# Performance work log

Measured on AMD Instinct MI355X. Metric: run time of the kernel, lower is better.

## Reference

```python
import jax, jax.numpy as jnp
import numpy as np

D = 512; PE = 64; H = 8; DH = 64; INNER = H * DH; FF = 4 * D
B = 2; L = 2048; K = 32; G = 128; LT = L + G
SCALE = DH ** -0.5


def _ln(x, g, b):
    m = jnp.mean(x, -1, keepdims=True)
    v = jnp.var(x, -1, keepdims=True)
    return (x - m) * jax.lax.rsqrt(v + 1e-5) * g + b


def _heads(x):
    b, n, _ = x.shape
    return x.reshape(b, n, H, DH).transpose(0, 2, 1, 3)


def _merge(x):
    b, _, n, _ = x.shape
    return x.transpose(0, 2, 1, 3).reshape(b, n, INNER)


def _cross(q_in, ctx, wq, wk, wv, wo, bo):
    Q = _heads(q_in @ wq); Kh = _heads(ctx @ wk); V = _heads(ctx @ wv)
    a = jax.nn.softmax(jnp.einsum('bhnd,bhmd->bhnm', Q, Kh) * SCALE, axis=-1)
    return _merge(jnp.einsum('bhnm,bhmd->bhnd', a, V)) @ wo + bo


def _ffn(x, w1, b1, w2, b2):
    return jax.nn.gelu(x @ w1 + b1, approximate=False) @ w2 + b2


def setup_inputs():
    key = jax.random.key(0)
    ks = jax.random.split(key, 40)
    w = lambda k, shape: jax.random.normal(k, shape, jnp.float32) * 0.02
    return dict(
        latents=jax.random.normal(ks[0], (B, LT, D), jnp.float32),
        rpe=jax.random.normal(ks[1], (B, L, K, PE), jnp.float32),
        distances=jax.random.uniform(ks[2], (B, L, K), jnp.float32) * 10.0,
        sn_g=jnp.ones((D,), jnp.float32), sn_b=jnp.zeros((D,), jnp.float32),
        la_wq=w(ks[3], (D, INNER)), la_wk=w(ks[4], (D + PE, INNER)), la_wv=w(ks[5], (D + PE, INNER)),
        la_wo=w(ks[6], (INNER, D)), la_bo=jnp.zeros((D,), jnp.float32),
        log_sigma=jnp.full((H,), float(np.log(3.0)), jnp.float32),
        scn_g=jnp.ones((D,), jnp.float32), scn_b=jnp.zeros((D,), jnp.float32),
        s2g_wq=w(ks[7], (D, INNER)), s2g_wk=w(ks[8], (D, INNER)), s2g_wv=w(ks[9], (D, INNER)),
        s2g_wo=w(ks[10], (INNER, D)), s2g_bo=jnp.zeros((D,), jnp.float32),
        gcn_g=jnp.ones((D,), jnp.float32), gcn_b=jnp.zeros((D,), jnp.float32),
        g2s_wq=w(ks[11], (D, INNER)), g2s_wk=w(ks[12], (D, INNER)), g2s_wv=w(ks[13], (D, INNER)),
        g2s_wo=w(ks[14], (INNER, D)), g2s_bo=jnp.zeros((D,), jnp.float32),
        gfn_g=jnp.ones((D,), jnp.float32), gfn_b=jnp.zeros((D,), jnp.float32),
        gff_w1=w(ks[15], (D, FF)), gff_b1=jnp.zeros((FF,), jnp.float32),
        gff_w2=w(ks[16], (FF, D)), gff_b2=jnp.zeros((D,), jnp.float32),
        sfn_g=jnp.ones((D,), jnp.float32), sfn_b=jnp.zeros((D,), jnp.float32),
        sff_w1=w(ks[17], (D, FF)), sff_b1=jnp.zeros((FF,), jnp.float32),
        sff_w2=w(ks[18], (FF, D)), sff_b2=jnp.zeros((D,), jnp.float32),
        topk_indices=jax.random.randint(ks[19], (B, L, K), 0, L),
        num_spatial=L,
    )


def _forward(latents, rpe, distances, sn_g, sn_b, la_wq, la_wk, la_wv, la_wo, la_bo, log_sigma,
             scn_g, scn_b, s2g_wq, s2g_wk, s2g_wv, s2g_wo, s2g_bo,
             gcn_g, gcn_b, g2s_wq, g2s_wk, g2s_wv, g2s_wo, g2s_bo,
             gfn_g, gfn_b, gff_w1, gff_b1, gff_w2, gff_b2,
             sfn_g, sfn_b, sff_w1, sff_b1, sff_w2, sff_b2,
             topk_indices, num_spatial):
    spatial = latents[:, :num_spatial]
    glob = latents[:, num_spatial:]
    b, l, _ = spatial.shape
    k = topk_indices.shape[-1]
    # 1) local self-attention: kNN gather + RPE concat + Gaussian distance bias
    xn = _ln(spatial, sn_g, sn_b)
    neighbors = jax.vmap(lambda xb, ib: xb[ib])(xn, topk_indices)      # [B, L, k, D]
    ctx = jnp.concatenate([neighbors, rpe], axis=-1)                   # [B, L, k, D+PE]
    Q = _heads(xn @ la_wq)                                             # [B, H, L, DH]
    Kt = (ctx @ la_wk).reshape(b, l, k, H, DH).transpose(0, 3, 1, 2, 4)
    Vt = (ctx @ la_wv).reshape(b, l, k, H, DH).transpose(0, 3, 1, 2, 4)
    attn = jnp.einsum('bhld,bhlkd->bhlk', Q, Kt) * SCALE
    sigma_sq = jnp.exp(2.0 * log_sigma)[None, :, None, None]           # sigma**2 per head
    attn = attn - (distances ** 2)[:, None] / (2.0 * sigma_sq)
    attn = jax.nn.softmax(attn, axis=-1)
    o = jnp.einsum('bhlk,bhlkd->bhld', attn, Vt)
    spatial = spatial + (_merge(o) @ la_wo + la_bo)
    # 2) spatial -> global, 3) global -> spatial, global FFN
    spatial = spatial + _cross(_ln(spatial, scn_g, scn_b), glob, s2g_wq, s2g_wk, s2g_wv, s2g_wo, s2g_bo)
    glob = glob + _cross(_ln(glob, gcn_g, gcn_b), spatial, g2s_wq, g2s_wk, g2s_wv, g2s_wo, g2s_bo)
    glob = glob + _ffn(_ln(glob, gfn_g, gfn_b), gff_w1, gff_b1, gff_w2, gff_b2)
    # 4) spatial FFN
    spatial = spatial + _ffn(_ln(spatial, sfn_g, sfn_b), sff_w1, sff_b1, sff_w2, sff_b2)
    return jnp.concatenate([spatial, glob], axis=1)


def reference(latents, rpe, distances, sn_g, sn_b, la_wq, la_wk, la_wv, la_wo, la_bo, log_sigma,
              scn_g, scn_b, s2g_wq, s2g_wk, s2g_wv, s2g_wo, s2g_bo,
              gcn_g, gcn_b, g2s_wq, g2s_wk, g2s_wv, g2s_wo, g2s_bo,
              gfn_g, gfn_b, gff_w1, gff_b1, gff_w2, gff_b2,
              sfn_g, sfn_b, sff_w1, sff_b1, sff_w2, sff_b2,
              topk_indices, num_spatial):
    return _forward(latents, rpe, distances, sn_g, sn_b, la_wq, la_wk, la_wv, la_wo, la_bo, log_sigma,
                    scn_g, scn_b, s2g_wq, s2g_wk, s2g_wv, s2g_wo, s2g_bo,
                    gcn_g, gcn_b, g2s_wq, g2s_wk, g2s_wv, g2s_wo, g2s_bo,
                    gfn_g, gfn_b, gff_w1, gff_b1, gff_w2, gff_b2,
                    sfn_g, sfn_b, sff_w1, sff_b1, sff_w2, sff_b2,
                    topk_indices, num_spatial)
```

## Files before the change

kernel.cpp:

```cpp
#include <hip/hip_runtime.h>
#include <math.h>

namespace {
constexpr int D = 512;
constexpr int PE = 64;
constexpr int H = 8;
constexpr int DH = 64;
constexpr int INNER = 512;
constexpr int FF = 2048;
constexpr int B = 2;
constexpr int L = 2048;
constexpr int KN = 32;
constexpr int G = 128;
constexpr int LT = L + G;
constexpr float SCALE = 0.125f;

typedef unsigned short u16;
typedef unsigned short u16x8 __attribute__((ext_vector_type(8)));
typedef float f32x4 __attribute__((ext_vector_type(4)));
typedef _Float16 h2 __attribute__((ext_vector_type(2)));

#if defined(__has_builtin)
#if __has_builtin(__builtin_amdgcn_fdot2)
#define HAVE_FDOT2 1
#endif
#endif

__device__ __forceinline__ u16 f2bf(float x) {
  union { float f; unsigned u; } v;
  v.f = x;
  unsigned r = v.u + 0x7fffu + ((v.u >> 16) & 1u);
  return (u16)(r >> 16);
}

__device__ __forceinline__ float bf2f(u16 x) {
  union { unsigned u; float f; } v;
  v.u = ((unsigned)x) << 16;
  return v.f;
}

__device__ __forceinline__ u16 f2h(float x) {
  _Float16 h = (_Float16)x;
  return *(u16*)&h;
}

__device__ __forceinline__ unsigned pack2bf(float a, float b) {
  return (unsigned)f2bf(a) | ((unsigned)f2bf(b) << 16);
}

__device__ __forceinline__ float gelu_exact(float x) {
  return 0.5f * x * (1.0f + erff(x * 0.7071067811865475f));
}

__device__ __forceinline__ f32x4 mfma_16x16x32_bf16(u16x8 a, u16x8 b, f32x4 c) {
  asm("v_mfma_f32_16x16x32_bf16 %0, %1, %2, %0" : "+v"(c) : "v"(a), "v"(b));
  return c;
}

__device__ __forceinline__ float dot2h(h2 a, h2 b, float c) {
#ifdef HAVE_FDOT2
  return __builtin_amdgcn_fdot2(a, b, c, false);
#else
  return c + (float)a[0] * (float)b[0] + (float)a[1] * (float)b[1];
#endif
}

__device__ __forceinline__ void gload_lds16(const u16* g, const u16* lds_base) {
  __builtin_amdgcn_global_load_lds(
      (const __attribute__((address_space(1))) unsigned int*)(uintptr_t)g,
      (__attribute__((address_space(3))) unsigned int*)(unsigned)(uintptr_t)lds_base,
      16, 0, 0);
}

__global__ __launch_bounds__(256) void split_kernel(const float* __restrict__ latents,
                                                    float* __restrict__ sp, float* __restrict__ gl) {
  int i = blockIdx.x * 256 + threadIdx.x;
  const int total = B * LT * D / 4;
  if (i >= total) return;
  float4 v = ((const float4*)latents)[i];
  int fi = i * 4;
  int d = fi % D;
  int row = fi / D;
  int l = row % LT;
  int b = row / LT;
  if (l < L) ((float4*)sp)[((size_t)(b * L + l) * D + d) / 4] = v;
  else ((float4*)gl)[((size_t)(b * G + (l - L)) * D + d) / 4] = v;
}

__global__ __launch_bounds__(256) void assemble_kernel(const float* __restrict__ sp,
                                                       const float* __restrict__ gl,
                                                       float* __restrict__ out) {
  int i = blockIdx.x * 256 + threadIdx.x;
  const int total = B * LT * D / 4;
  if (i >= total) return;
  int fi = i * 4;
  int d = fi % D;
  int row = fi / D;
  int l = row % LT;
  int b = row / LT;
  float4 v;
  if (l < L) v = ((const float4*)sp)[((size_t)(b * L + l) * D + d) / 4];
  else v = ((const float4*)gl)[((size_t)(b * G + (l - L)) * D + d) / 4];
  ((float4*)out)[i] = v;
}

__global__ __launch_bounds__(256) void ln_kernel(const float* __restrict__ in,
                                                 const float* __restrict__ gw,
                                                 const float* __restrict__ bw,
                                                 u16* __restrict__ out) {
  int row = blockIdx.x;
  int t = threadIdx.x;
  const float* x = in + (size_t)row * D;
  float2 v = ((const float2*)x)[t];
  float s = v.x + v.y;
  float sq = v.x * v.x + v.y * v.y;
#pragma unroll
  for (int m = 1; m < 64; m <<= 1) {
    s += __shfl_xor(s, m, 64);
    sq += __shfl_xor(sq, m, 64);
  }
  __shared__ float ss[4], s2[4];
  int w = t >> 6;
  if ((t & 63) == 0) { ss[w] = s; s2[w] = sq; }
  __syncthreads();
  s = ss[0] + ss[1] + ss[2] + ss[3];
  sq = s2[0] + s2[1] + s2[2] + s2[3];
  float mean = s * (1.0f / D);
  float var = sq * (1.0f / D) - mean * mean;
  float rs = rsqrtf(var + 1e-5f);
  float2 gv = ((const float2*)gw)[t];
  float2 bv = ((const float2*)bw)[t];
  float ox = (v.x - mean) * rs * gv.x + bv.x;
  float oy = (v.y - mean) * rs * gv.y + bv.y;
  ((unsigned*)(out + (size_t)row * D))[t] = pack2bf(ox, oy);
}

__global__ __launch_bounds__(256) void cvt_bf16_kernel(const float* __restrict__ in,
                                                       u16* __restrict__ out, int n4) {
  int i = blockIdx.x * 256 + threadIdx.x;
  if (i >= n4) return;
  float4 v = ((const float4*)in)[i];
  ushort4 o;
  o.x = f2bf(v.x); o.y = f2bf(v.y); o.z = f2bf(v.z); o.w = f2bf(v.w);
  ((ushort4*)out)[i] = o;
}

struct WtJob { const float* src; u16* dst; int K; int N; int off; int dstride; };
struct WtJobs { WtJob j[16]; };

__global__ __launch_bounds__(256) void wt_convert_kernel(WtJobs jobs) {
  __shared__ float tile[32][33];
  int bid = blockIdx.x;
  int e = 0;
#pragma unroll
  for (int i = 1; i < 16; ++i) if (bid >= jobs.j[i].off) e = i;
  const WtJob& J = jobs.j[e];
  int ti = bid - J.off;
  int tiles_n = J.N >> 5;
  int tk = ti / tiles_n, tn = ti - tk * tiles_n;
  int t = threadIdx.x;
  int r = t >> 3, c4 = (t & 7) * 4;
  float4 v = *(const float4*)&J.src[(size_t)(tk * 32 + r) * J.N + tn * 32 + c4];
  tile[r][c4 + 0] = v.x; tile[r][c4 + 1] = v.y; tile[r][c4 + 2] = v.z; tile[r][c4 + 3] = v.w;
  __syncthreads();
  int r2 = t >> 3, k4 = (t & 7) * 4;
  ushort4 o;
  o.x = f2bf(tile[k4 + 0][r2]);
  o.y = f2bf(tile[k4 + 1][r2]);
  o.z = f2bf(tile[k4 + 2][r2]);
  o.w = f2bf(tile[k4 + 3][r2]);
  *(ushort4*)&J.dst[(size_t)(tn * 32 + r2) * J.dstride + tk * 32 + k4] = o;
}

__global__ __launch_bounds__(256) void comp_qt_kernel(const float* __restrict__ wq,
                                                      const float* __restrict__ wkb,
                                                      u16* __restrict__ out) {
  int h = blockIdx.x, ct = blockIdx.y;
  __shared__ float wk_s[64][68];
  __shared__ float wq_s[64][68];
  int t = threadIdx.x;
  int r = t >> 4, c4 = (t & 15) * 4;
#pragma unroll
  for (int i = 0; i < 4; ++i) {
    int rr = r + i * 16;
    *(float4*)&wk_s[rr][c4] = *(const float4*)&wkb[(size_t)rr * INNER + h * DH + c4];
    *(float4*)&wq_s[rr][c4] = *(const float4*)&wq[(size_t)(ct * 64 + rr) * INNER + h * DH + c4];
  }
  __syncthreads();
  int p = t >> 2, cb = (t & 3) * 16;
  float acc[16] = {};
  for (int d = 0; d < 64; ++d) {
    float a = wk_s[p][d];
#pragma unroll
    for (int j = 0; j < 16; ++j) acc[j] += a * wq_s[cb + j][d];
  }
  for (int j = 0; j < 16; ++j)
    out[(size_t)(h * 64 + p) * INNER + ct * 64 + cb + j] = f2bf(acc[j]);
}

__global__ __launch_bounds__(256) void comp_wo_kernel(const float* __restrict__ la_wo,
                                                      const float* __restrict__ wvb,
                                                      u16* __restrict__ WO2t) {
  int h = blockIdx.x, jt = blockIdx.y;
  __shared__ float lo_s[64][68];
  __shared__ float wv_s[64][68];
  int t = threadIdx.x;
  int r = t >> 4, c4 = (t & 15) * 4;
#pragma unroll
  for (int i = 0; i < 4; ++i) {
    int rr = r + i * 16;
    *(float4*)&lo_s[rr][c4] = *(const float4*)&la_wo[(size_t)(h * DH + rr) * D + jt * 64 + c4];
    *(float4*)&wv_s[rr][c4] = *(const float4*)&wvb[(size_t)rr * INNER + h * DH + c4];
  }
  __syncthreads();
  int j = t >> 2, pb = (t & 3) * 16;
  float acc[16] = {};
  for (int d = 0; d < 64; ++d) {
    float a = lo_s[d][j];
#pragma unroll
    for (int i = 0; i < 16; ++i) acc[i] += a * wv_s[pb + i][d];
  }
  for (int i = 0; i < 16; ++i)
    WO2t[(size_t)(jt * 64 + j) * 1024 + 512 + h * DH + pb + i] = f2bf(acc[i]);
}

struct WSet { const u16* W[4]; void* out[4]; };

template <int BM, int BN>
__global__ __launch_bounds__(256) void gemm_v3_kernel(const u16* __restrict__ A, WSet gs,
                                                      const float* __restrict__ bias,
                                                      const float* __restrict__ res,
                                                      u16* __restrict__ out_bf,
                                                      int M, int K, int N, int act, unsigned obf) {
  constexpr int FM = BM / 32;
  constexpr int FN = BN / 32;
  __shared__ u16 As[2][BM * 64];
  __shared__ u16 Bs[2][BN * 64];
  int t = threadIdx.x;
  int wave = __builtin_amdgcn_readfirstlane(t >> 6);
  int lane = t & 63;
  int wr = wave >> 1, wc = wave & 1;
  int row16 = lane & 15, katom = lane >> 4;
  int bm = blockIdx.y * BM, bn = blockIdx.x * BN;
  const u16* W = gs.W[blockIdx.z];
  void* outp = gs.out[blockIdx.z];
  unsigned obz = (obf >> (blockIdx.z * 2)) & 3u;
  int srow = lane >> 3;
  int sg = lane & 7;
  int swz = row16 & 7;
  f32x4 acc[FM][FN] = {};

  auto stage = [&](int buf, int kb) {
#pragma unroll
    for (int c = 0; c < BM / 32; ++c) {
      int rowbase = wave * (BM / 4) + c * 8;
      int row = rowbase + srow;
      int gsrc = sg ^ (row & 7);
      gload_lds16(&A[(size_t)(bm + row) * K + kb + gsrc * 8], &As[buf][rowbase * 64]);
    }
#pragma unroll
    for (int c = 0; c < BN / 32; ++c) {
      int rowbase = wave * (BN / 4) + c * 8;
      int row = rowbase + srow;
      int gsrc = sg ^ (row & 7);
      gload_lds16(&W[(size_t)(bn + row) * K + kb + gsrc * 8], &Bs[buf][rowbase * 64]);
    }
  };

  stage(0, 0);
  __syncthreads();
  int nk = K >> 6;
  int cur = 0;
  for (int ti = 0; ti < nk; ++ti) {
    u16x8 af[2][FM], bf[2][FN];
#pragma unroll
    for (int kk = 0; kk < 2; ++kk) {
#pragma unroll
      for (int m = 0; m < FM; ++m) {
        int r = wr * (BM / 2) + m * 16 + row16;
        af[kk][m] = *(u16x8*)&As[cur][r * 64 + ((kk * 4 + katom) ^ swz) * 8];
      }
#pragma unroll
      for (int n = 0; n < FN; ++n) {
        int r = wc * (BN / 2) + n * 16 + row16;
        bf[kk][n] = *(u16x8*)&Bs[cur][r * 64 + ((kk * 4 + katom) ^ swz) * 8];
      }
    }
    __builtin_amdgcn_sched_barrier(0);
    if (ti + 1 < nk) stage(cur ^ 1, (ti + 1) << 6);
#pragma unroll
    for (int kk = 0; kk < 2; ++kk)
#pragma unroll
      for (int m = 0; m < FM; ++m)
#pragma unroll
        for (int n = 0; n < FN; ++n)
          acc[m][n] = mfma_16x16x32_bf16(af[kk][m], bf[kk][n], acc[m][n]);
    __syncthreads();
    cur ^= 1;
  }
#pragma unroll
  for (int m = 0; m < FM; ++m) {
    int row = bm + wr * (BM / 2) + m * 16 + katom * 4;
#pragma unroll
    for (int n = 0; n < FN; ++n) {
      int col = bn + wc * (BN / 2) + n * 16 + row16;
      float bsv = bias ? bias[col] : 0.f;
#pragma unroll
      for (int r = 0; r < 4; ++r) {
        float v = acc[m][n][r] + bsv;
        if (act) v = gelu_exact(v);
        size_t oi = (size_t)(row + r) * N + col;
        if (res) v += res[oi];
        if (obz == 1) ((u16*)outp)[oi] = f2bf(v);
        else if (obz == 3) ((u16*)outp)[oi] = f2h(v);
        else {
          ((float*)outp)[oi] = v;
          if (obz == 2) out_bf[oi] = f2bf(v);
        }
      }
    }
  }
}

__global__ __launch_bounds__(256) void local_attn2_kernel(
    const u16* __restrict__ Qh, const u16* __restrict__ Kh, const u16* __restrict__ Vh,
    const u16* __restrict__ TQh, const float* __restrict__ rpe, const float* __restrict__ dist,
    const int* __restrict__ idx, const float* __restrict__ lsig, u16* __restrict__ OA) {
  int blk = blockIdx.x;
  int b = blk >> 11;
  int t = threadIdx.x;
  __shared__ _Float16 q_s[INNER];
  __shared__ float tq_s[INNER];
  __shared__ float rpe_s[KN][68];
  __shared__ float a_s[H][KN + 1];
  __shared__ float ar_s[H][PE + 2];
  __shared__ int idx_s[KN];
  __shared__ float dist_s[KN];
  __shared__ float sig_s[H];
  size_t row = (size_t)blk;
  {
    unsigned qp = ((const unsigned*)(Qh + row * INNER))[t];
    q_s[2 * t] = (_Float16)bf2f((u16)qp);
    q_s[2 * t + 1] = (_Float16)bf2f((u16)(qp >> 16));
    unsigned tp = ((const unsigned*)(TQh + row * INNER))[t];
    tq_s[2 * t] = bf2f((u16)tp);
    tq_s[2 * t + 1] = bf2f((u16)(tp >> 16));
  }
  {
    const float* rp = rpe + row * (KN * PE);
    int k = t >> 3, p0 = (t & 7) * 8;
    *(float4*)&rpe_s[k][p0] = *(const float4*)&rp[k * PE + p0];
    *(float4*)&rpe_s[k][p0 + 4] = *(const float4*)&rp[k * PE + p0 + 4];
  }
  if (t < KN) {
    idx_s[t] = idx[row * KN + t];
    dist_s[t] = dist[row * KN + t];
  }
  if (t < H) sig_s[t] = expf(2.0f * lsig[t]);
  __syncthreads();
  {
    int h = t >> 5, k = t & 31;
    int rr = idx_s[k];
    const u16* krow = Kh + ((size_t)(b * L + rr)) * INNER + h * DH;
    float acc = 0.f;
#pragma unroll
    for (int i = 0; i < 8; ++i) {
      u16x8 kv = *(const u16x8*)&krow[i * 8];
      u16x8 qv = *(const u16x8*)&q_s[h * DH + i * 8];
      const h2* kk = (const h2*)&kv;
      const h2* qq = (const h2*)&qv;
      acc = dot2h(kk[0], qq[0], acc);
      acc = dot2h(kk[1], qq[1], acc);
      acc = dot2h(kk[2], qq[2], acc);
      acc = dot2h(kk[3], qq[3], acc);
    }
    float accr = 0.f;
    const float* tqh = tq_s + h * DH;
#pragma unroll
    for (int p = 0; p < PE; p += 4) {
      float4 r4 = *(float4*)&rpe_s[k][p];
      float4 t4 = *(const float4*)&tqh[p];
      accr += r4.x * t4.x + r4.y * t4.y + r4.z * t4.z + r4.w * t4.w;
    }
    float dd = dist_s[k];
    float logit = SCALE * (acc + accr) - dd * dd / (2.0f * sig_s[h]);
    float mx = logit;
#pragma unroll
    for (int m = 1; m < 32; m <<= 1) mx = fmaxf(mx, __shfl_xor(mx, m, 64));
    float e = expf(logit - mx);
    float sum = e;
#pragma unroll
    for (int m = 1; m < 32; m <<= 1) sum += __shfl_xor(sum, m, 64);
    a_s[h][k] = e / sum;
  }
  __syncthreads();
  {
    int hh = t >> 6, p = t & 63;
    float acc0 = 0.f, acc1 = 0.f;
#pragma unroll
    for (int k = 0; k < KN; ++k) {
      float rv = rpe_s[k][p];
      acc0 += a_s[hh][k] * rv;
      acc1 += a_s[hh + 4][k] * rv;
    }
    ar_s[hh][p] = acc0;
    ar_s[hh + 4][p] = acc1;
  }
  __syncthreads();
  {
    int h0 = t >> 5;
    h2 o2;
    o2[0] = (_Float16)0.f;
    o2[1] = (_Float16)0.f;
#pragma unroll 8
    for (int k = 0; k < KN; ++k) {
      unsigned vv = *(const unsigned*)&Vh[((size_t)(b * L + idx_s[k])) * INNER + 2 * t];
      h2 v2 = *(h2*)&vv;
      _Float16 ah = (_Float16)a_s[h0][k];
      h2 a2;
      a2[0] = ah; a2[1] = ah;
      o2 = a2 * v2 + o2;
    }
    ((unsigned*)&OA[row * 1024])[t] = pack2bf((float)o2[0], (float)o2[1]);
    int p0 = 2 * (t & 31);
    ((unsigned*)&OA[row * 1024 + 512])[t] = pack2bf(ar_s[t >> 5][p0], ar_s[t >> 5][p0 + 1]);
  }
}

__global__ __launch_bounds__(256) void s2g_attn_kernel(const float* __restrict__ Q2,
                                                       const float* __restrict__ Kg,
                                                       const float* __restrict__ Vg,
                                                       u16* __restrict__ O) {
  int l0 = blockIdx.x * 32;
  int h = blockIdx.y;
  int b = blockIdx.z;
  int t = threadIdx.x;
  __shared__ float q_s[32][68];
  __shared__ float kv_s[128][68];
  __shared__ float lg[32][132];
  for (int i = t; i < 512; i += 256) {
    int r = i >> 4, c = (i & 15) * 4;
    *(float4*)&q_s[r][c] = *(const float4*)&Q2[((size_t)(b * L + l0 + r)) * INNER + h * DH + c];
  }
  for (int i = t; i < 2048; i += 256) {
    int r = i >> 4, c = (i & 15) * 4;
    *(float4*)&kv_s[r][c] = *(const float4*)&Kg[((size_t)(b * G + r)) * INNER + h * DH + c];
  }
  __syncthreads();
  int q = t >> 3, mg = t & 7;
  {
    float lv[16];
    float lmax = -1e30f;
#pragma unroll
    for (int i = 0; i < 16; ++i) {
      int m = mg + 8 * i;
      float acc = 0.f;
#pragma unroll
      for (int d = 0; d < DH; d += 4) {
        float4 kk = *(float4*)&kv_s[m][d];
        acc += kk.x * q_s[q][d] + kk.y * q_s[q][d + 1] + kk.z * q_s[q][d + 2] + kk.w * q_s[q][d + 3];
      }
      lv[i] = acc * SCALE;
      lmax = fmaxf(lmax, lv[i]);
    }
#pragma unroll
    for (int msk = 1; msk < 8; msk <<= 1) lmax = fmaxf(lmax, __shfl_xor(lmax, msk, 64));
    float lsum = 0.f;
#pragma unroll
    for (int i = 0; i < 16; ++i) {
      float e = expf(lv[i] - lmax);
      lv[i] = e;
      lsum += e;
    }
#pragma unroll
    for (int msk = 1; msk < 8; msk <<= 1) lsum += __shfl_xor(lsum, msk, 64);
    float inv = 1.0f / lsum;
#pragma unroll
    for (int i = 0; i < 16; ++i) lg[q][mg + 8 * i] = lv[i] * inv;
  }
  __syncthreads();
  for (int i = t; i < 2048; i += 256) {
    int r = i >> 4, c = (i & 15) * 4;
    *(float4*)&kv_s[r][c] = *(const float4*)&Vg[((size_t)(b * G + r)) * INNER + h * DH + c];
  }
  __syncthreads();
  {
    int dg = t & 7;
    float o[8] = {};
    for (int m = 0; m < G; ++m) {
      float w = lg[q][m];
      float4 v0 = *(float4*)&kv_s[m][dg * 8];
      float4 v1 = *(float4*)&kv_s[m][dg * 8 + 4];
      o[0] += w * v0.x; o[1] += w * v0.y; o[2] += w * v0.z; o[3] += w * v0.w;
      o[4] += w * v1.x; o[5] += w * v1.y; o[6] += w * v1.z; o[7] += w * v1.w;
    }
    size_t base = ((size_t)(b * L + l0 + q)) * INNER + h * DH + dg * 8;
    ushort4 s0, s1;
    s0.x = f2bf(o[0]); s0.y = f2bf(o[1]); s0.z = f2bf(o[2]); s0.w = f2bf(o[3]);
    s1.x = f2bf(o[4]); s1.y = f2bf(o[5]); s1.z = f2bf(o[6]); s1.w = f2bf(o[7]);
    *(ushort4*)&O[base] = s0;
    *(ushort4*)&O[base + 4] = s1;
  }
}

__global__ __launch_bounds__(256) void g2s_logits_kernel(const u16* __restrict__ QGh,
                                                         const u16* __restrict__ KBh,
                                                         float* __restrict__ LG) {
  __shared__ u16 Qs[128 * 72];
  __shared__ u16 Ks[128 * 72];
  int nt = blockIdx.x, h = blockIdx.y, b = blockIdx.z;
  int t = threadIdx.x;
  int wave = t >> 6, lane = t & 63;
  int row16 = lane & 15, katom = lane >> 4;
#pragma unroll
  for (int i = 0; i < 4; ++i) {
    int row = (t >> 3) + i * 32;
    int cg = t & 7;
    *(u16x8*)&Qs[row * 72 + cg * 8] =
        *(const u16x8*)&QGh[((size_t)(b * G + row)) * INNER + h * DH + cg * 8];
    *(u16x8*)&Ks[row * 72 + cg * 8] =
        *(const u16x8*)&KBh[((size_t)(b * L + nt * 128 + row)) * INNER + h * DH + cg * 8];
  }
  __syncthreads();
  f32x4 acc[2][8] = {};
#pragma unroll
  for (int kk = 0; kk < 2; ++kk) {
    u16x8 af[2], bf[8];
#pragma unroll
    for (int qt = 0; qt < 2; ++qt)
      af[qt] = *(u16x8*)&Qs[(wave * 32 + qt * 16 + row16) * 72 + kk * 32 + katom * 8];
#pragma unroll
    for (int nm = 0; nm < 8; ++nm)
      bf[nm] = *(u16x8*)&Ks[(nm * 16 + row16) * 72 + kk * 32 + katom * 8];
#pragma unroll
    for (int qt = 0; qt < 2; ++qt)
#pragma unroll
      for (int nm = 0; nm < 8; ++nm) acc[qt][nm] = mfma_16x16x32_bf16(af[qt], bf[nm], acc[qt][nm]);
  }
#pragma unroll
  for (int qt = 0; qt < 2; ++qt) {
    int g = wave * 32 + qt * 16 + katom * 4;
#pragma unroll
    for (int nm = 0; nm < 8; ++nm) {
      int m = nt * 128 + nm * 16 + row16;
#pragma unroll
      for (int r = 0; r < 4; ++r)
        LG[(((size_t)(b * H + h) * G) + g + r) * L + m] = acc[qt][nm][r] * SCALE;
    }
  }
}

__global__ __launch_bounds__(256) void g2s_softmax_kernel(const float* __restrict__ LG,
                                                          u16* __restrict__ WG) {
  int g = blockIdx.x & (G - 1);
  int b = blockIdx.x >> 7;
  int t = threadIdx.x;
  int w = t >> 6, lane = t & 63;
  __shared__ float red[8];
  for (int h = 0; h < H; ++h) {
    size_t base = (((size_t)(b * H + h) * G) + g) * L;
    float4 lo = *(const float4*)&LG[base + t * 8];
    float4 hi = *(const float4*)&LG[base + t * 8 + 4];
    float mx = fmaxf(fmaxf(fmaxf(lo.x, lo.y), fmaxf(lo.z, lo.w)),
                     fmaxf(fmaxf(hi.x, hi.y), fmaxf(hi.z, hi.w)));
#pragma unroll
    for (int m = 1; m < 64; m <<= 1) mx = fmaxf(mx, __shfl_xor(mx, m, 64));
    if (lane == 0) red[w] = mx;
    __syncthreads();
    mx = fmaxf(fmaxf(red[0], red[1]), fmaxf(red[2], red[3]));
    float e[8];
    e[0] = expf(lo.x - mx); e[1] = expf(lo.y - mx); e[2] = expf(lo.z - mx); e[3] = expf(lo.w - mx);
    e[4] = expf(hi.x - mx); e[5] = expf(hi.y - mx); e[6] = expf(hi.z - mx); e[7] = expf(hi.w - mx);
    float sum = e[0] + e[1] + e[2] + e[3] + e[4] + e[5] + e[6] + e[7];
#pragma unroll
    for (int m = 1; m < 64; m <<= 1) sum += __shfl_xor(sum, m, 64);
    if (lane == 0) red[4 + w] = sum;
    __syncthreads();
    float inv = 1.0f / (red[4] + red[5] + red[6] + red[7]);
    ushort4 o0, o1;
    o0.x = f2bf(e[0] * inv); o0.y = f2bf(e[1] * inv); o0.z = f2bf(e[2] * inv); o0.w = f2bf(e[3] * inv);
    o1.x = f2bf(e[4] * inv); o1.y = f2bf(e[5] * inv); o1.z = f2bf(e[6] * inv); o1.w = f2bf(e[7] * inv);
    *(ushort4*)&WG[base + t * 8] = o0;
    *(ushort4*)&WG[base + t * 8 + 4] = o1;
    __syncthreads();
  }
}

__global__ __launch_bounds__(256) void g2s_vt_kernel(const u16* __restrict__ VBh,
                                                     u16* __restrict__ Vt) {
  __shared__ u16 tile[32][36];
  int mt = blockIdx.x, ct = blockIdx.y, b = blockIdx.z;
  int t = threadIdx.x;
  int r = t >> 3, c4 = (t & 7) * 4;
  *(ushort4*)&tile[r][c4] =
      *(const ushort4*)&VBh[((size_t)(b * L + mt * 32 + r)) * INNER + ct * 32 + c4];
  __syncthreads();
  int r2 = t >> 3, m4 = (t & 7) * 4;
  int c = ct * 32 + r2;
  int h = c >> 6, d = c & 63;
  ushort4 o;
  o.x = tile[m4 + 0][r2]; o.y = tile[m4 + 1][r2]; o.z = tile[m4 + 2][r2]; o.w = tile[m4 + 3][r2];
  *(ushort4*)&Vt[(((size_t)(b * H + h) * DH) + d) * L + mt * 32 + m4] = o;
}

__global__ __launch_bounds__(256) void g2s_pv_kernel(const u16* __restrict__ WG,
                                                     const u16* __restrict__ Vt,
                                                     float* __restrict__ Opart) {
  __shared__ u16 Ws[128 * 40];
  __shared__ u16 Vs[64 * 40];
  int s = blockIdx.x, h = blockIdx.y, b = blockIdx.z;
  int t = threadIdx.x;
  int wave = t >> 6, lane = t & 63;
  int row16 = lane & 15, katom = lane >> 4;
  int r0 = t >> 2, cg = t & 3;
  size_t wbase = ((size_t)(b * H + h) * G) * L;
  size_t vbase = ((size_t)(b * H + h) * DH) * L;
  f32x4 acc[2][4] = {};
  for (int it = 0; it < 8; ++it) {
    int m0 = s * 256 + it * 32;
    u16x8 w0 = *(const u16x8*)&WG[wbase + (size_t)r0 * L + m0 + cg * 8];
    u16x8 w1 = *(const u16x8*)&WG[wbase + (size_t)(r0 + 64) * L + m0 + cg * 8];
    u16x8 v0 = *(const u16x8*)&Vt[vbase + (size_t)(t >> 2) * L + m0 + cg * 8];
    __syncthreads();
    *(u16x8*)&Ws[r0 * 40 + cg * 8] = w0;
    *(u16x8*)&Ws[(r0 + 64) * 40 + cg * 8] = w1;
    *(u16x8*)&Vs[(t >> 2) * 40 + cg * 8] = v0;
    __syncthreads();
    u16x8 af[2], bf[4];
#pragma unroll
    for (int qt = 0; qt < 2; ++qt)
      af[qt] = *(u16x8*)&Ws[(wave * 32 + qt * 16 + row16) * 40 + katom * 8];
#pragma unroll
    for (int nd = 0; nd < 4; ++nd)
      bf[nd] = *(u16x8*)&Vs[(nd * 16 + row16) * 40 + katom * 8];
#pragma unroll
    for (int qt = 0; qt < 2; ++qt)
#pragma unroll
      for (int nd = 0; nd < 4; ++nd) acc[qt][nd] = mfma_16x16x32_bf16(af[qt], bf[nd], acc[qt][nd]);
  }
  size_t obase = (((size_t)(b * H + h) * 8) + s) * G * DH;
#pragma unroll
  for (int qt = 0; qt < 2; ++qt) {
    int g = wave * 32 + qt * 16 + katom * 4;
#pragma unroll
    for (int nd = 0; nd < 4; ++nd) {
      int d = nd * 16 + row16;
#pragma unroll
      for (int r = 0; r < 4; ++r) Opart[obase + (size_t)(g + r) * DH + d] = acc[qt][nd][r];
    }
  }
}

__global__ __launch_bounds__(256) void g2s_combine_kernel(const float* __restrict__ Opart,
                                                          u16* __restrict__ OGh) {
  int g = blockIdx.x & (G - 1);
  int b = blockIdx.x >> 7;
  int t = threadIdx.x;
  int h = t >> 5, d0 = (t & 31) * 2;
  float o0 = 0.f, o1 = 0.f;
#pragma unroll
  for (int s = 0; s < 8; ++s) {
    const float* p = Opart + ((((size_t)(b * H + h) * 8) + s) * G + g) * DH + d0;
    o0 += p[0];
    o1 += p[1];
  }
  *(unsigned*)&OGh[((size_t)(b * G + g)) * INNER + h * DH + d0] = pack2bf(o0, o1);
}

}

extern "C" void kernel_launch(void* const* d_in, const int* in_sizes, int n_in,
                              void* d_out, int out_size, void* d_ws, size_t ws_size,
                              hipStream_t stream) {
  (void)in_sizes; (void)n_in; (void)out_size; (void)ws_size;
  const float* latents = (const float*)d_in[0];
  const float* rpe = (const float*)d_in[1];
  const float* dist = (const float*)d_in[2];
  const float* sn_g = (const float*)d_in[3];
  const float* sn_b = (const float*)d_in[4];
  const float* la_wq = (const float*)d_in[5];
  const float* la_wk = (const float*)d_in[6];
  const float* la_wv = (const float*)d_in[7];
  const float* la_wo = (const float*)d_in[8];
  const float* la_bo = (const float*)d_in[9];
  const float* log_sigma = (const float*)d_in[10];
  const float* scn_g = (const float*)d_in[11];
  const float* scn_b = (const float*)d_in[12];
  const float* s2g_wq = (const float*)d_in[13];
  const float* s2g_wk = (const float*)d_in[14];
  const float* s2g_wv = (const float*)d_in[15];
  const float* s2g_wo = (const float*)d_in[16];
  const float* s2g_bo = (const float*)d_in[17];
  const float* gcn_g = (const float*)d_in[18];
  const float* gcn_b = (const float*)d_in[19];
  const float* g2s_wq = (const float*)d_in[20];
  const float* g2s_wk = (const float*)d_in[21];
  const float* g2s_wv = (const float*)d_in[22];
  const float* g2s_wo = (const float*)d_in[23];
  const float* g2s_bo = (const float*)d_in[24];
  const float* gfn_g = (const float*)d_in[25];
  const float* gfn_b = (const float*)d_in[26];
  const float* gff_w1 = (const float*)d_in[27];
  const float* gff_b1 = (const float*)d_in[28];
  const float* gff_w2 = (const float*)d_in[29];
  const float* gff_b2 = (const float*)d_in[30];
  const float* sfn_g = (const float*)d_in[31];
  const float* sfn_b = (const float*)d_in[32];
  const float* sff_w1 = (const float*)d_in[33];
  const float* sff_b1 = (const float*)d_in[34];
  const float* sff_w2 = (const float*)d_in[35];
  const float* sff_b2 = (const float*)d_in[36];
  const int* topk = (const int*)d_in[37];
  const float* wkb = la_wk + (size_t)D * INNER;
  const float* wvb = la_wv + (size_t)D * INNER;

  char* wsb = (char*)d_ws;
  size_t off = 0;
  auto alloc = [&](size_t bytes) {
    char* p = wsb + off;
    off += (bytes + 255) & ~(size_t)255;
    return p;
  };
  const size_t SPn = (size_t)B * L * D;
  const size_t GLn = (size_t)B * G * D;
  float* SP = (float*)alloc(SPn * 4);
  float* GL = (float*)alloc(GLn * 4);
  float* QB = (float*)alloc(SPn * 4);
  float* KB = (float*)alloc(SPn * 4);
  float* VB = (float*)alloc(SPn * 4);
  float* S1 = (float*)alloc(SPn * 4);
  float* S2 = (float*)alloc(SPn * 4);
  float* G1 = (float*)alloc(GLn * 4);
  float* G2 = (float*)alloc(GLn * 4);
  float* QG = (float*)alloc(GLn * 4);
  float* KG = (float*)alloc(GLn * 4);
  float* VG = (float*)alloc(GLn * 4);
  u16* XNh = (u16*)alloc(SPn * 2);
  u16* OBh = (u16*)alloc(SPn * 2);
  u16* S2h = (u16*)alloc(SPn * 2);
  u16* HSh = (u16*)alloc((size_t)B * L * FF * 2);
  u16* GLh = (u16*)alloc(GLn * 2);
  u16* GNh = (u16*)alloc(GLn * 2);
  u16* OGh = (u16*)alloc(GLn * 2);
  u16* HGh = (u16*)alloc((size_t)B * G * FF * 2);
  const size_t SQ = 512 * 512, BIG = 512 * 2048;
  u16* WT = (u16*)alloc((12 * SQ + 4 * BIG) * 2);
  u16* la_wq_t = WT + 0 * SQ;
  u16* la_wk_t = WT + 1 * SQ;
  u16* la_wv_t = WT + 2 * SQ;
  u16* s2g_wq_t = WT + 4 * SQ;
  u16* s2g_wk_t = WT + 5 * SQ;
  u16* s2g_wv_t = WT + 6 * SQ;
  u16* s2g_wo_t = WT + 7 * SQ;
  u16* g2s_wq_t = WT + 8 * SQ;
  u16* g2s_wk_t = WT + 9 * SQ;
  u16* g2s_wv_t = WT + 10 * SQ;
  u16* g2s_wo_t = WT + 11 * SQ;
  u16* gff1_t = WT + 12 * SQ;
  u16* gff2_t = WT + 12 * SQ + BIG;
  u16* sff1_t = WT + 12 * SQ + 2 * BIG;
  u16* sff2_t = WT + 12 * SQ + 3 * BIG;
  u16* WQTt = (u16*)alloc(SQ * 2);
  u16* WO2t = (u16*)alloc(512 * 1024 * 2);

  u16* lkh = (u16*)KB;
  u16* lvh = (u16*)KB + SPn;
  u16* ltqh = (u16*)VB;
  u16* lqh = (u16*)VB + SPn;
  u16* OA = (u16*)QB;

  float* LG = KB;
  u16* WG = (u16*)S1;
  u16* KBh = (u16*)QB;
  u16* VBh = (u16*)QB + SPn;
  u16* QGh = HSh;
  u16* Vt = HSh + GLn;
  float* Opart = (float*)(HSh + GLn + (size_t)B * H * DH * L);

  const int threads = 256;
  int nsplit = (B * LT * D / 4 + 255) / 256;

  split_kernel<<<nsplit, threads, 0, stream>>>(latents, SP, GL);

  {
    WtJobs jobs;
    auto set = [&](int i, const float* s, u16* d, int K, int N, int offv, int dstride) {
      jobs.j[i].src = s; jobs.j[i].dst = d; jobs.j[i].K = K; jobs.j[i].N = N;
      jobs.j[i].off = offv; jobs.j[i].dstride = dstride;
    };
    int o = 0;
    set(0, la_wq, la_wq_t, 512, 512, o, 512); o += 256;
    set(1, la_wk, la_wk_t, 512, 512, o, 512); o += 256;
    set(2, la_wv, la_wv_t, 512, 512, o, 512); o += 256;
    set(3, la_wo, WO2t, 512, 512, o, 1024); o += 256;
    set(4, s2g_wq, s2g_wq_t, 512, 512, o, 512); o += 256;
    set(5, s2g_wk, s2g_wk_t, 512, 512, o, 512); o += 256;
    set(6, s2g_wv, s2g_wv_t, 512, 512, o, 512); o += 256;
    set(7, s2g_wo, s2g_wo_t, 512, 512, o, 512); o += 256;
    set(8, g2s_wq, g2s_wq_t, 512, 512, o, 512); o += 256;
    set(9, g2s_wk, g2s_wk_t, 512, 512, o, 512); o += 256;
    set(10, g2s_wv, g2s_wv_t, 512, 512, o, 512); o += 256;
    set(11, g2s_wo, g2s_wo_t, 512, 512, o, 512); o += 256;
    set(12, gff_w1, gff1_t, 512, 2048, o, 512); o += 1024;
    set(13, gff_w2, gff2_t, 2048, 512, o, 2048); o += 1024;
    set(14, sff_w1, sff1_t, 512, 2048, o, 512); o += 1024;
    set(15, sff_w2, sff2_t, 2048, 512, o, 2048); o += 1024;
    wt_convert_kernel<<<o, threads, 0, stream>>>(jobs);
  }
  comp_qt_kernel<<<dim3(8, 8), threads, 0, stream>>>(la_wq, wkb, WQTt);
  comp_wo_kernel<<<dim3(8, 8), threads, 0, stream>>>(la_wo, wvb, WO2t);

  auto gemm = [&](const u16* A, const u16* Wt, const float* bias, const float* res,
                  void* out, int M, int K, int N, int act, unsigned obf, u16* out_bf) {
    WSet gs{};
    gs.W[0] = Wt; gs.out[0] = out;
    if (N >= 1024)
      gemm_v3_kernel<64, 128><<<dim3(N / 128, M / 64, 1), threads, 0, stream>>>(
          A, gs, bias, res, out_bf, M, K, N, act, obf);
    else
      gemm_v3_kernel<64, 64><<<dim3(N / 64, M / 64, 1), threads, 0, stream>>>(
          A, gs, bias, res, out_bf, M, K, N, act, obf);
  };
  auto gemm_multi = [&](const u16* A, const u16* W0, const u16* W1, const u16* W2, const u16* W3,
                        void* o0, void* o1, void* o2, void* o3, int nw, int M, int K, int N,
                        unsigned obf) {
    WSet gs{};
    gs.W[0] = W0; gs.W[1] = W1; gs.W[2] = W2; gs.W[3] = W3;
    gs.out[0] = o0; gs.out[1] = o1; gs.out[2] = o2; gs.out[3] = o3;
    gemm_v3_kernel<64, 64><<<dim3(N / 64, M / 64, nw), threads, 0, stream>>>(
        A, gs, nullptr, nullptr, nullptr, M, K, N, 0, obf);
  };

  ln_kernel<<<B * L, threads, 0, stream>>>(SP, sn_g, sn_b, XNh);
  gemm_multi(XNh, la_wq_t, la_wk_t, la_wv_t, WQTt, lqh, lkh, lvh, ltqh, 4, B * L, D, INNER,
             1u | (3u << 2) | (3u << 4) | (1u << 6));
  local_attn2_kernel<<<B * L, threads, 0, stream>>>(lqh, lkh, lvh, ltqh, rpe, dist, topk,
                                                    log_sigma, OA);
  gemm(OA, WO2t, la_bo, SP, S1, B * L, 1024, D, 0, 0, nullptr);

  ln_kernel<<<B * L, threads, 0, stream>>>(S1, scn_g, scn_b, XNh);
  gemm(XNh, s2g_wq_t, nullptr, nullptr, QB, B * L, D, INNER, 0, 0, nullptr);
  cvt_bf16_kernel<<<(int)(GLn / 4 + 255) / 256, threads, 0, stream>>>(GL, GLh, (int)(GLn / 4));
  gemm_multi(GLh, s2g_wk_t, s2g_wv_t, nullptr, nullptr, KG, VG, nullptr, nullptr, 2, B * G, D, INNER, 0);
  s2g_attn_kernel<<<dim3(L / 32, H, B), threads, 0, stream>>>(QB, KG, VG, OBh);
  gemm(OBh, s2g_wo_t, s2g_bo, S1, S2, B * L, INNER, D, 0, 2, S2h);

  ln_kernel<<<B * G, threads, 0, stream>>>(GL, gcn_g, gcn_b, GNh);
  gemm(GNh, g2s_wq_t, nullptr, nullptr, QGh, B * G, D, INNER, 0, 1, nullptr);
  gemm_multi(S2h, g2s_wk_t, g2s_wv_t, nullptr, nullptr, KBh, VBh, nullptr, nullptr, 2, B * L, D, INNER,
             1u | (1u << 2));
  g2s_vt_kernel<<<dim3(L / 32, INNER / 32, B), threads, 0, stream>>>(VBh, Vt);
  g2s_logits_kernel<<<dim3(L / 128, H, B), threads, 0, stream>>>(QGh, KBh, LG);
  g2s_softmax_kernel<<<B * G, threads, 0, stream>>>(LG, WG);
  g2s_pv_kernel<<<dim3(8, H, B), threads, 0, stream>>>(WG, Vt, Opart);
  g2s_combine_kernel<<<B * G, threads, 0, stream>>>(Opart, OGh);
  gemm(OGh, g2s_wo_t, g2s_bo, GL, G1, B * G, INNER, D, 0, 0, nullptr);

  ln_kernel<<<B * G, threads, 0, stream>>>(G1, gfn_g, gfn_b, GNh);
  gemm(GNh, gff1_t, gff_b1, nullptr, HGh, B * G, D, FF, 1, 1, nullptr);
  gemm(HGh, gff2_t, gff_b2, G1, G2, B * G, FF, D, 0, 0, nullptr);

  ln_kernel<<<B * L, threads, 0, stream>>>(S2, sfn_g, sfn_b, XNh);
  gemm(XNh, sff1_t, sff_b1, nullptr, HSh, B * L, D, FF, 1, 1, nullptr);
  gemm(HSh, sff2_t, sff_b2, S2, S1, B * L, FF, D, 0, 0, nullptr);

  assemble_kernel<<<nsplit, threads, 0, stream>>>(S1, G2, (float*)d_out);
}
```

Before: 348.0 us.

## Rewrite spatial-to-global attention with bf16 MFMA and bf16 Q/K/V projections

Replaces the scalar fp32 s2g attention kernel with an MFMA-based kernel. It computes QK^T and PV using 16x16x32 bf16 matrix instructions, with a cross-wave softmax reduction done in shared memory and V transposed into LDS. The Q, K and V projection GEMMs now write bf16 instead of fp32, which halves their output traffic and the attention kernel's loads. The cost is lower precision in the attention probabilities and in Q/K/V.

New measurement: 322.4 us. 1.08x faster.

```diff
diff --git a/kernel.cpp b/kernel.cpp
--- a/kernel.cpp
+++ b/kernel.cpp
@@ -427,79 +427,151 @@
   }
 }
 
-__global__ __launch_bounds__(256) void s2g_attn_kernel(const float* __restrict__ Q2,
-                                                       const float* __restrict__ Kg,
-                                                       const float* __restrict__ Vg,
-                                                       u16* __restrict__ O) {
-  int l0 = blockIdx.x * 32;
+__global__ __launch_bounds__(256) void s2g_attn_mfma_kernel(const u16* __restrict__ Qh,
+                                                            const u16* __restrict__ Kg,
+                                                            const u16* __restrict__ Vg,
+                                                            u16* __restrict__ O) {
+  int l0 = blockIdx.x * 64;
   int h = blockIdx.y;
   int b = blockIdx.z;
   int t = threadIdx.x;
-  __shared__ float q_s[32][68];
-  __shared__ float kv_s[128][68];
-  __shared__ float lg[32][132];
+  int wave = __builtin_amdgcn_readfirstlane(t >> 6);
+  int lane = t & 63;
+  int wr = wave >> 1, wc = wave & 1;
+  int row16 = lane & 15, katom = lane >> 4;
+  __shared__ u16 Qs[64 * 72];
+  __shared__ u16 Ks[128 * 72];
+  __shared__ u16 Ps[64 * 136];
+  __shared__ float redm[2][64], reds[2][64];
+  u16* VT = Ks;
+
   for (int i = t; i < 512; i += 256) {
-    int r = i >> 4, c = (i & 15) * 4;
-    *(float4*)&q_s[r][c] = *(const float4*)&Q2[((size_t)(b * L + l0 + r)) * INNER + h * DH + c];
-  }
-  for (int i = t; i < 2048; i += 256) {
-    int r = i >> 4, c = (i & 15) * 4;
-    *(float4*)&kv_s[r][c] = *(const float4*)&Kg[((size_t)(b * G + r)) * INNER + h * DH + c];
-  }
-  __syncthreads();
-  int q = t >> 3, mg = t & 7;
+    int r = i >> 3, s = i & 7;
+    *(u16x8*)&Qs[r * 72 + s * 8] = *(const u16x8*)&Qh[((size_t)(b * L + l0 + r)) * INNER + h * DH + s * 8];
+  }
+  for (int i = t; i < 1024; i += 256) {
+    int r = i >> 3, s = i & 7;
+    *(u16x8*)&Ks[r * 72 + s * 8] = *(const u16x8*)&Kg[((size_t)(b * G + r)) * INNER + h * DH + s * 8];
+  }
+  __syncthreads();
+
+  f32x4 acc[2][4] = {};
+#pragma unroll
+  for (int kk = 0; kk < 2; ++kk) {
+    u16x8 af[2], bf[4];
+#pragma unroll
+    for (int m = 0; m < 2; ++m)
+      af[m] = *(u16x8*)&Qs[(wr * 32 + m * 16 + row16) * 72 + kk * 32 + katom * 8];
+#pragma unroll
+    for (int n = 0; n < 4; ++n)
+      bf[n] = *(u16x8*)&Ks[(wc * 64 + n * 16 + row16) * 72 + kk * 32 + katom * 8];
+#pragma unroll
+    for (int m = 0; m < 2; ++m)
+#pragma unroll
+      for (int n = 0; n < 4; ++n) acc[m][n] = mfma_16x16x32_bf16(af[m], bf[n], acc[m][n]);
+  }
+#pragma unroll
+  for (int m = 0; m < 2; ++m)
+#pragma unroll
+    for (int n = 0; n < 4; ++n)
+#pragma unroll
+      for (int r = 0; r < 4; ++r) acc[m][n][r] *= SCALE;
+
+  float mx[2][4];
+#pragma unroll
+  for (int m = 0; m < 2; ++m)
+#pragma unroll
+    for (int r = 0; r < 4; ++r) {
+      float v = fmaxf(fmaxf(acc[m][0][r], acc[m][1][r]), fmaxf(acc[m][2][r], acc[m][3][r]));
+#pragma unroll
+      for (int msk = 1; msk < 16; msk <<= 1) v = fmaxf(v, __shfl_xor(v, msk, 64));
+      mx[m][r] = v;
+    }
+  if (row16 == 0) {
+#pragma unroll
+    for (int m = 0; m < 2; ++m)
+#pragma unroll
+      for (int r = 0; r < 4; ++r) redm[wc][wr * 32 + m * 16 + katom * 4 + r] = mx[m][r];
+  }
+  __syncthreads();
+
   {
-    float lv[16];
-    float lmax = -1e30f;
-#pragma unroll
-    for (int i = 0; i < 16; ++i) {
-      int m = mg + 8 * i;
-      float acc = 0.f;
-#pragma unroll
-      for (int d = 0; d < DH; d += 4) {
-        float4 kk = *(float4*)&kv_s[m][d];
-        acc += kk.x * q_s[q][d] + kk.y * q_s[q][d + 1] + kk.z * q_s[q][d + 2] + kk.w * q_s[q][d + 3];
+    int m = t >> 1, ch = t & 1;
+    const u16* vrow = Vg + ((size_t)(b * G + m)) * INNER + h * DH + ch * 32;
+#pragma unroll
+    for (int j = 0; j < 8; ++j) {
+      ushort4 v = *(const ushort4*)&vrow[j * 4];
+      int c = ch * 32 + j * 4;
+      VT[(c + 0) * 136 + m] = v.x;
+      VT[(c + 1) * 136 + m] = v.y;
+      VT[(c + 2) * 136 + m] = v.z;
+      VT[(c + 3) * 136 + m] = v.w;
+    }
+  }
+
+  float sm[2][4];
+#pragma unroll
+  for (int m = 0; m < 2; ++m)
+#pragma unroll
+    for (int r = 0; r < 4; ++r) {
+      int qi = wr * 32 + m * 16 + katom * 4 + r;
+      float gm = fmaxf(redm[0][qi], redm[1][qi]);
+      float s = 0.f;
+#pragma unroll
+      for (int n = 0; n < 4; ++n) {
+        float e = expf(acc[m][n][r] - gm);
+        acc[m][n][r] = e;
+        s += e;
       }
-      lv[i] = acc * SCALE;
-      lmax = fmaxf(lmax, lv[i]);
-    }
-#pragma unroll
-    for (int msk = 1; msk < 8; msk <<= 1) lmax = fmaxf(lmax, __shfl_xor(lmax, msk, 64));
-    float lsum = 0.f;
-#pragma unroll
-    for (int i = 0; i < 16; ++i) {
-      float e = expf(lv[i] - lmax);
-      lv[i] = e;
-      lsum += e;
-    }
-#pragma unroll
-    for (int msk = 1; msk < 8; msk <<= 1) lsum += __shfl_xor(lsum, msk, 64);
-    float inv = 1.0f / lsum;
-#pragma unroll
-    for (int i = 0; i < 16; ++i) lg[q][mg + 8 * i] = lv[i] * inv;
-  }
-  __syncthreads();
-  for (int i = t; i < 2048; i += 256) {
-    int r = i >> 4, c = (i & 15) * 4;
-    *(float4*)&kv_s[r][c] = *(const float4*)&Vg[((size_t)(b * G + r)) * INNER + h * DH + c];
-  }
-  __syncthreads();
-  {
-    int dg = t & 7;
-    float o[8] = {};
-    for (int m = 0; m < G; ++m) {
-      float w = lg[q][m];
-      float4 v0 = *(float4*)&kv_s[m][dg * 8];
-      float4 v1 = *(float4*)&kv_s[m][dg * 8 + 4];
-      o[0] += w * v0.x; o[1] += w * v0.y; o[2] += w * v0.z; o[3] += w * v0.w;
-      o[4] += w * v1.x; o[5] += w * v1.y; o[6] += w * v1.z; o[7] += w * v1.w;
-    }
-    size_t base = ((size_t)(b * L + l0 + q)) * INNER + h * DH + dg * 8;
-    ushort4 s0, s1;
-    s0.x = f2bf(o[0]); s0.y = f2bf(o[1]); s0.z = f2bf(o[2]); s0.w = f2bf(o[3]);
-    s1.x = f2bf(o[4]); s1.y = f2bf(o[5]); s1.z = f2bf(o[6]); s1.w = f2bf(o[7]);
-    *(ushort4*)&O[base] = s0;
-    *(ushort4*)&O[base + 4] = s1;
+#pragma unroll
+      for (int msk = 1; msk < 16; msk <<= 1) s += __shfl_xor(s, msk, 64);
+      sm[m][r] = s;
+    }
+  if (row16 == 0) {
+#pragma unroll
+    for (int m = 0; m < 2; ++m)
+#pragma unroll
+      for (int r = 0; r < 4; ++r) reds[wc][wr * 32 + m * 16 + katom * 4 + r] = sm[m][r];
+  }
+  __syncthreads();
+
+#pragma unroll
+  for (int m = 0; m < 2; ++m)
+#pragma unroll
+    for (int r = 0; r < 4; ++r) {
+      int qi = wr * 32 + m * 16 + katom * 4 + r;
+      float inv = 1.0f / (reds[0][qi] + reds[1][qi]);
+#pragma unroll
+      for (int n = 0; n < 4; ++n)
+        Ps[qi * 136 + wc * 64 + n * 16 + row16] = f2bf(acc[m][n][r] * inv);
+    }
+  __syncthreads();
+
+  f32x4 oacc[2][2] = {};
+#pragma unroll
+  for (int kk = 0; kk < 4; ++kk) {
+    u16x8 pa[2], vb[2];
+#pragma unroll
+    for (int m = 0; m < 2; ++m)
+      pa[m] = *(u16x8*)&Ps[(wr * 32 + m * 16 + row16) * 136 + kk * 32 + katom * 8];
+#pragma unroll
+    for (int n = 0; n < 2; ++n)
+      vb[n] = *(u16x8*)&VT[(wc * 32 + n * 16 + row16) * 136 + kk * 32 + katom * 8];
+#pragma unroll
+    for (int m = 0; m < 2; ++m)
+#pragma unroll
+      for (int n = 0; n < 2; ++n) oacc[m][n] = mfma_16x16x32_bf16(pa[m], vb[n], oacc[m][n]);
+  }
+#pragma unroll
+  for (int m = 0; m < 2; ++m) {
+    int q = wr * 32 + m * 16 + katom * 4;
+#pragma unroll
+    for (int n = 0; n < 2; ++n) {
+      int d = wc * 32 + n * 16 + row16;
+#pragma unroll
+      for (int r = 0; r < 4; ++r)
+        O[((size_t)(b * L + l0 + q + r)) * INNER + h * DH + d] = f2bf(oacc[m][n][r]);
+    }
   }
 }
 
@@ -769,6 +841,10 @@
   u16* lqh = (u16*)VB + SPn;
   u16* OA = (u16*)QB;
 
+  u16* QBh = (u16*)QB;
+  u16* KGh = (u16*)KG;
+  u16* VGh = (u16*)VG;
+
   float* LG = KB;
   u16* WG = (u16*)S1;
   u16* KBh = (u16*)QB;
@@ -839,10 +915,11 @@
   gemm(OA, WO2t, la_bo, SP, S1, B * L, 1024, D, 0, 0, nullptr);
 
   ln_kernel<<<B * L, threads, 0, stream>>>(S1, scn_g, scn_b, XNh);
-  gemm(XNh, s2g_wq_t, nullptr, nullptr, QB, B * L, D, INNER, 0, 0, nullptr);
+  gemm(XNh, s2g_wq_t, nullptr, nullptr, QBh, B * L, D, INNER, 0, 1, nullptr);
   cvt_bf16_kernel<<<(int)(GLn / 4 + 255) / 256, threads, 0, stream>>>(GL, GLh, (int)(GLn / 4));
-  gemm_multi(GLh, s2g_wk_t, s2g_wv_t, nullptr, nullptr, KG, VG, nullptr, nullptr, 2, B * G, D, INNER, 0);
-  s2g_attn_kernel<<<dim3(L / 32, H, B), threads, 0, stream>>>(QB, KG, VG, OBh);
+  gemm_multi(GLh, s2g_wk_t, s2g_wv_t, nullptr, nullptr, KGh, VGh, nullptr, nullptr, 2, B * G, D, INNER,
+             1u | (1u << 2));
+  s2g_attn_mfma_kernel<<<dim3(L / 64, H, B), threads, 0, stream>>>(QBh, KGh, VGh, OBh);
   gemm(OBh, s2g_wo_t, s2g_bo, S1, S2, B * L, INNER, D, 0, 2, S2h);
 
   ln_kernel<<<B * G, threads, 0, stream>>>(GL, gcn_g, gcn_b, GNh);
```
